# Kernel tuning notes

Measured on AMD Instinct MI355X. Metric: run time of the kernel, lower is better.

## Reference

```python
import jax, jax.numpy as jnp
import numpy as np

N = 50000      # nodes per type
E = 800000     # edges per relation
D = 128        # input feature dim
H = 128        # hidden_channels


def setup_inputs() -> dict:
    key = jax.random.key(0)
    ks = jax.random.split(key, 20)
    f = lambda k, shp: jax.random.normal(k, shp, dtype=jnp.float32) * 0.05
    inp = {
        "x_ligand": jax.random.normal(ks[0], (N, D), dtype=jnp.float32),
        "x_protein": jax.random.normal(ks[1], (N, D), dtype=jnp.float32),
        "ei_lp": jax.random.randint(ks[2], (2, E), 0, N, dtype=jnp.int64),
        "ei_pp": jax.random.randint(ks[3], (2, E), 0, N, dtype=jnp.int64),
        "ei_ll": jax.random.randint(ks[4], (2, E), 0, N, dtype=jnp.int64),
        "Wl_lp": f(ks[5], (D, H)), "bl_lp": f(ks[6], (H,)), "Wr_lp": f(ks[7], (D, H)),
        "Wl_pp": f(ks[8], (D, H)), "bl_pp": f(ks[9], (H,)), "Wr_pp": f(ks[10], (D, H)),
        "Wl_ll": f(ks[11], (D, H)), "bl_ll": f(ks[12], (H,)), "Wr_ll": f(ks[13], (D, H)),
        "W_out": f(ks[14], (H, 1)), "b_out": f(ks[15], (1,)),
    }
    return inp


def _sage(x_src, x_dst, edge_index, Wl, bl, Wr):
    # PyG SAGEConv: mean-aggregate neighbor (src) features onto dst, then
    # out = lin_l(agg) + lin_r(x_dst)  (lin_l has bias, lin_r does not)
    src, dst = edge_index[0], edge_index[1]
    n_dst = x_dst.shape[0]
    msgs = x_src[src]                                      # [E, D] gather
    s = jax.ops.segment_sum(msgs, dst, num_segments=n_dst) # [N_dst, D]
    cnt = jax.ops.segment_sum(jnp.ones((edge_index.shape[1],), x_src.dtype),
                              dst, num_segments=n_dst)     # [N_dst]
    agg = s / jnp.maximum(cnt, 1.0)[:, None]               # mean, 0 if isolated
    return agg @ Wl + bl + x_dst @ Wr


def reference(x_ligand, x_protein, ei_lp, ei_pp, ei_ll,
              Wl_lp, bl_lp, Wr_lp, Wl_pp, bl_pp, Wr_pp,
              Wl_ll, bl_ll, Wr_ll, W_out, b_out):
    # HeteroConv: sum contributions per destination node type
    protein_out = (_sage(x_ligand, x_protein, ei_lp, Wl_lp, bl_lp, Wr_lp)
                   + _sage(x_protein, x_protein, ei_pp, Wl_pp, bl_pp, Wr_pp))
    ligand_out = _sage(x_ligand, x_ligand, ei_ll, Wl_ll, bl_ll, Wr_ll)
    # relu per node type; only ligand is used downstream
    lig = jax.nn.relu(ligand_out).mean(axis=0)             # [H]
    _ = jax.nn.relu(protein_out)                           # computed in original
    return lig @ W_out + b_out                             # [1]
```

## Files before the change

### kernel.cpp

```cpp
#include <hip/hip_runtime.h>
#include <hip/hip_bf16.h>

#define DIM 128
#define EPB 4096
#define NRBIN 1024
#define RCAP 1280

typedef __attribute__((ext_vector_type(8))) short bf16x8;
typedef __attribute__((ext_vector_type(4))) float f32x4;
typedef __attribute__((ext_vector_type(4))) short short4v;
typedef __attribute__((ext_vector_type(4))) int int4v;

__device__ inline unsigned short f2bf(float f) {
  union { float f; unsigned u; } v; v.f = f;
  return (unsigned short)((v.u + 0x7FFFu + ((v.u >> 16) & 1u)) >> 16);
}
__device__ inline float lo_f(unsigned u) {
  union { unsigned u; float f; } v; v.u = u << 16; return v.f;
}
__device__ inline float hi_f(unsigned u) {
  union { unsigned u; float f; } v; v.u = u & 0xFFFF0000u; return v.f;
}

__global__ __launch_bounds__(256) void prep_part_kernel(
    const int* __restrict__ ei, unsigned* __restrict__ chunkbuf,
    int* __restrict__ startsT, int* __restrict__ countsT, int E, int nchunk,
    const float* __restrict__ x, short* __restrict__ A,
    const float* __restrict__ Wl, const float* __restrict__ Wr,
    short* __restrict__ Bpack, int nnodes, int mpad, int xb) {
  __shared__ unsigned uns[EPB];
  __shared__ unsigned srt[EPB];
  __shared__ int lhist[NRBIN];
  __shared__ int lstart[NRBIN];
  __shared__ int tsum[256];
  const int tid = threadIdx.x;
  const int bid = blockIdx.x;

  if (bid >= nchunk) {
    if (bid < nchunk + xb) {
      int t = (bid - nchunk) * 256 + tid;
      int node = t >> 5;
      if (node >= mpad) return;
      int c = (t & 31) * 4;
      short4v o = (short4v){0, 0, 0, 0};
      if (node < nnodes) {
        float4 v = *reinterpret_cast<const float4*>(x + (size_t)node * DIM + c);
        o.x = (short)f2bf(v.x); o.y = (short)f2bf(v.y);
        o.z = (short)f2bf(v.z); o.w = (short)f2bf(v.w);
      }
      *reinterpret_cast<short4v*>(A + (size_t)node * DIM + c) = o;
    } else {
      int t = (bid - nchunk - xb) * 256 + tid;
      if (t >= 4096) return;
      int lane = t & 63, nt = (t >> 6) & 7, ks = t >> 9;
      int c = nt * 16 + (lane & 15);
      int kb = ks * 32 + ((lane >> 4) << 3);
      bf16x8 o;
#pragma unroll
      for (int j = 0; j < 8; ++j) {
        int k = kb + j;
        float v = (k < DIM) ? Wl[k * DIM + c] : Wr[(k - DIM) * DIM + c];
        o[j] = (short)f2bf(v);
      }
      reinterpret_cast<bf16x8*>(Bpack)[(ks * 8 + nt) * 64 + lane] = o;
    }
    return;
  }

  const int chunk = bid;
  const int base = chunk * EPB;
  const int count = min(EPB, E - base);

#pragma unroll
  for (int r = 0; r < NRBIN / 256; ++r) lhist[tid + 256 * r] = 0;
  __syncthreads();

  for (int r = 0; r < EPB / 1024; ++r) {
    int i = r * 1024 + tid * 4;
    if (i + 3 < count) {
      int4 s4 = *reinterpret_cast<const int4*>(ei + base + i);
      int4 d4 = *reinterpret_cast<const int4*>(ei + E + base + i);
      int ss[4] = {s4.x, s4.y, s4.z, s4.w};
      int dd[4] = {d4.x, d4.y, d4.z, d4.w};
#pragma unroll
      for (int k = 0; k < 4; ++k) {
        unsigned reg = (unsigned)dd[k] >> 6;
        uns[i + k] = (reg << 22) | ((unsigned)(dd[k] & 63) << 16) | (unsigned)ss[k];
        atomicAdd(&lhist[reg], 1);
      }
    } else {
      for (int k = 0; k < 4; ++k) {
        if (i + k < count) {
          int s = ei[base + i + k], d = ei[E + base + i + k];
          unsigned reg = (unsigned)d >> 6;
          uns[i + k] = (reg << 22) | ((unsigned)(d & 63) << 16) | (unsigned)s;
          atomicAdd(&lhist[reg], 1);
        }
      }
    }
  }
  __syncthreads();

  int h0 = lhist[tid * 4], h1 = lhist[tid * 4 + 1];
  int h2 = lhist[tid * 4 + 2], h3 = lhist[tid * 4 + 3];
  int local = h0 + h1 + h2 + h3;
  tsum[tid] = local;
  __syncthreads();
  for (int o = 1; o < 256; o <<= 1) {
    int t = (tid >= o) ? tsum[tid - o] : 0;
    __syncthreads();
    tsum[tid] += t;
    __syncthreads();
  }
  int tb = tsum[tid] - local;
  lstart[tid * 4]     = tb;
  lstart[tid * 4 + 1] = tb + h0;
  lstart[tid * 4 + 2] = tb + h0 + h1;
  lstart[tid * 4 + 3] = tb + h0 + h1 + h2;
  lhist[tid * 4] = 0; lhist[tid * 4 + 1] = 0;
  lhist[tid * 4 + 2] = 0; lhist[tid * 4 + 3] = 0;
  __syncthreads();

  for (int i = tid; i < count; i += 256) {
    unsigned e = uns[i];
    unsigned reg = e >> 22;
    int pos = lstart[reg] + atomicAdd(&lhist[reg], 1);
    srt[pos] = e;
  }
  __syncthreads();

  for (int r = 0; r < EPB / 1024; ++r) {
    int i = r * 1024 + tid * 4;
    if (i + 3 < count) {
      int4v v = {(int)srt[i], (int)srt[i + 1], (int)srt[i + 2], (int)srt[i + 3]};
      *reinterpret_cast<int4v*>(chunkbuf + (size_t)chunk * EPB + i) = v;
    } else {
      for (int k = 0; k < 4; ++k)
        if (i + k < count) chunkbuf[(size_t)chunk * EPB + i + k] = srt[i + k];
    }
  }
  for (int r = tid; r < NRBIN; r += 256) {
    startsT[(size_t)chunk * NRBIN + r] = lstart[r];
    countsT[(size_t)chunk * NRBIN + r] = lhist[r];
  }
}

__global__ __launch_bounds__(256) void compact_kernel(
    const unsigned* __restrict__ chunkbuf, const int* __restrict__ startsT,
    const int* __restrict__ countsT, int nchunk, unsigned* __restrict__ csr,
    int* __restrict__ cnt, int* __restrict__ off) {
  __shared__ unsigned raw[RCAP];
  __shared__ unsigned srt[RCAP];
  __shared__ int h[64];
  __shared__ int start[64];
  __shared__ int tsum[256];
  const int region = blockIdx.x;
  const int tid = threadIdx.x;

  int cn = 0, st = 0;
  if (tid < nchunk) {
    cn = countsT[(size_t)tid * NRBIN + region];
    st = startsT[(size_t)tid * NRBIN + region];
  }
  tsum[tid] = cn;
  __syncthreads();
  for (int o = 1; o < 256; o <<= 1) {
    int t = (tid >= o) ? tsum[tid - o] : 0;
    __syncthreads();
    tsum[tid] += t;
    __syncthreads();
  }
  const int pfx = tsum[tid] - cn;
  int total = min(tsum[255], RCAP);

  const unsigned* src = chunkbuf + (size_t)tid * EPB + st;
  for (int j = 0; j < cn && pfx + j < RCAP; ++j) raw[pfx + j] = src[j];
  if (tid < 64) h[tid] = 0;
  __syncthreads();

  for (int i = tid; i < total; i += 256) atomicAdd(&h[(raw[i] >> 16) & 63], 1);
  __syncthreads();
  if (tid == 0) {
    int s = 0;
    for (int i = 0; i < 64; ++i) { start[i] = s; s += h[i]; }
  }
  __syncthreads();
  if (tid < 64) {
    int node = region * 64 + tid;
    cnt[node] = h[tid];
    off[node] = region * RCAP + start[tid];
    h[tid] = 0;
  }
  __syncthreads();
  for (int i = tid; i < total; i += 256) {
    unsigned e = raw[i];
    int d = (e >> 16) & 63;
    int pos = start[d] + atomicAdd(&h[d], 1);
    srt[pos] = e & 0xFFFFu;
  }
  __syncthreads();
  for (int i = tid; i < total; i += 256) csr[(size_t)region * RCAP + i] = srt[i];
}

__global__ __launch_bounds__(512) void aggmm_kernel(
    const int* __restrict__ cnt, const int* __restrict__ off,
    const unsigned* __restrict__ bucket, const short* __restrict__ A,
    const short* __restrict__ Bpack, const float* __restrict__ bl,
    float* __restrict__ partial, int nnodes) {
  __shared__ short a_lds[64 * 256];
  const int tid = threadIdx.x;
  const int wave = tid >> 6;
  const int lane = tid & 63;
  const int mt = blockIdx.x;
  const unsigned* xs = reinterpret_cast<const unsigned*>(A) + lane;

  for (int n = 0; n < 8; ++n) {
    const int row = wave * 8 + n;
    const int node = mt * 64 + row;
    float l0 = 0.f, h0 = 0.f, l1 = 0.f, h1 = 0.f;
    float r = 0.f;
    if (node < nnodes) {
      const int deg  = __builtin_amdgcn_readfirstlane(cnt[node]);
      const int base = __builtin_amdgcn_readfirstlane(off[node]);
      unsigned ent = (lane < deg) ? bucket[base + lane] : 0u;
      const int dcap = min(deg, 64);
      int j = 0;
      for (; j + 15 < dcap; j += 16) {
        unsigned u[16];
#pragma unroll
        for (int k = 0; k < 16; ++k) {
          int s = __builtin_amdgcn_readlane((int)ent, j + k);
          u[k] = xs[(size_t)s * 64];
        }
#pragma unroll
        for (int k = 0; k < 16; ++k) {
          if (k & 1) { l1 += lo_f(u[k]); h1 += hi_f(u[k]); }
          else       { l0 += lo_f(u[k]); h0 += hi_f(u[k]); }
        }
      }
      for (; j + 7 < dcap; j += 8) {
        unsigned u[8];
#pragma unroll
        for (int k = 0; k < 8; ++k) {
          int s = __builtin_amdgcn_readlane((int)ent, j + k);
          u[k] = xs[(size_t)s * 64];
        }
#pragma unroll
        for (int k = 0; k < 8; ++k) {
          if (k & 1) { l1 += lo_f(u[k]); h1 += hi_f(u[k]); }
          else       { l0 += lo_f(u[k]); h0 += hi_f(u[k]); }
        }
      }
      for (; j < dcap; ++j) {
        int s = __builtin_amdgcn_readlane((int)ent, j);
        unsigned u0 = xs[(size_t)s * 64];
        l0 += lo_f(u0); h0 += hi_f(u0);
      }
      for (; j < deg; ++j) {
        int s = __builtin_amdgcn_readfirstlane((int)bucket[base + j]);
        unsigned u0 = xs[(size_t)s * 64];
        l0 += lo_f(u0); h0 += hi_f(u0);
      }
      r = 1.0f / fmaxf((float)deg, 1.0f);
    }
    const unsigned o = (unsigned)f2bf((l0 + l1) * r) |
                       ((unsigned)f2bf((h0 + h1) * r) << 16);
    int byte = ((row * 512 + (lane >> 2) * 16) ^ ((row & 7) << 4)) + (lane & 3) * 4;
    *reinterpret_cast<unsigned*>(reinterpret_cast<char*>(a_lds) + byte) = o;
  }

#pragma unroll
  for (int rr = 0; rr < 2; ++rr) {
    int i = tid + 512 * rr;
    int row = i >> 4;
    int kc = 16 + (i & 15);
    bf16x8 v = *reinterpret_cast<const bf16x8*>(
        A + (size_t)(mt * 64 + row) * DIM + (kc - 16) * 8);
    int byte = (row * 512 + kc * 16) ^ ((row & 7) << 4);
    *reinterpret_cast<bf16x8*>(reinterpret_cast<char*>(a_lds) + byte) = v;
  }
  __syncthreads();

  f32x4 acc[4];
#pragma unroll
  for (int nt = 0; nt < 4; ++nt) acc[nt] = (f32x4){0.f, 0.f, 0.f, 0.f};

  const int stripe = wave >> 1;
  const int ntbase = (wave & 1) * 4;
  const int arow = stripe * 16 + (lane & 15);
  const int kgrp = lane >> 4;
  const bf16x8* Bp = reinterpret_cast<const bf16x8*>(Bpack);

#pragma unroll
  for (int ks = 0; ks < 8; ++ks) {
    int byte = (arow * 512 + (ks * 32 + kgrp * 8) * 2) ^ ((arow & 7) << 4);
    bf16x8 a = *reinterpret_cast<const bf16x8*>(reinterpret_cast<char*>(a_lds) + byte);
#pragma unroll
    for (int nt = 0; nt < 4; ++nt) {
      bf16x8 b = Bp[(ks * 8 + ntbase + nt) * 64 + lane];
      acc[nt] = __builtin_amdgcn_mfma_f32_16x16x32_bf16(a, b, acc[nt], 0, 0, 0);
    }
  }

  const int col16 = lane & 15;
  const int rowbase = mt * 64 + stripe * 16 + kgrp * 4;
#pragma unroll
  for (int nt = 0; nt < 4; ++nt) {
    const int c = (ntbase + nt) * 16 + col16;
    const float bb = bl[c];
    float s = 0.f;
#pragma unroll
    for (int rg = 0; rg < 4; ++rg) {
      float v = fmaxf(acc[nt][rg] + bb, 0.f);
      s += (rowbase + rg < nnodes) ? v : 0.f;
    }
    s += __shfl_xor(s, 16);
    s += __shfl_xor(s, 32);
    if (kgrp == 0) partial[((size_t)mt * 4 + stripe) * DIM + c] = s;
  }
}

__global__ __launch_bounds__(256) void red1_kernel(
    const float* __restrict__ partial, int nrows, float* __restrict__ red) {
  __shared__ float tmp[128];
  const int c = threadIdx.x & 127;
  const int half = threadIdx.x >> 7;
  const int chunk = (nrows + 127) / 128;
  const int r0 = blockIdx.x * chunk;
  const int r1 = min(r0 + chunk, nrows);
  float s = 0.f;
  for (int r = r0 + half; r < r1; r += 2) s += partial[(size_t)r * DIM + c];
  if (half) tmp[c] = s;
  __syncthreads();
  if (!half) red[(size_t)blockIdx.x * DIM + c] = s + tmp[c];
}

__global__ __launch_bounds__(256) void red2_kernel(
    const float* __restrict__ red, const float* __restrict__ Wout,
    const float* __restrict__ bout, float* __restrict__ out, int nnodes) {
  __shared__ float tmp[128];
  __shared__ float prod[128];
  const int c = threadIdx.x & 127;
  const int half = threadIdx.x >> 7;
  float s = 0.f;
  for (int r = half; r < 128; r += 2) s += red[(size_t)r * DIM + c];
  if (half) tmp[c] = s;
  __syncthreads();
  if (!half) prod[c] = (s + tmp[c]) * Wout[c];
  __syncthreads();
  if (threadIdx.x == 0) {
    float v = 0.f;
    for (int i = 0; i < 128; ++i) v += prod[i];
    out[0] = v / (float)nnodes + bout[0];
  }
}

extern "C" void kernel_launch(void* const* d_in, const int* in_sizes, int n_in,
                              void* d_out, int out_size, void* d_ws, size_t ws_size,
                              hipStream_t stream) {
  const float* x    = (const float*)d_in[0];
  const int*   ei   = (const int*)d_in[4];
  const float* Wl   = (const float*)d_in[11];
  const float* bl   = (const float*)d_in[12];
  const float* Wr   = (const float*)d_in[13];
  const float* Wout = (const float*)d_in[14];
  const float* bout = (const float*)d_in[15];

  const int nnodes = in_sizes[0] / DIM;
  const int E = in_sizes[4] / 2;
  const int mtiles = (nnodes + 63) / 64;
  const int mpad = mtiles * 64;
  const int nchunk = (E + EPB - 1) / EPB;

  unsigned* chunkbuf = (unsigned*)d_ws;
  int*      startsT  = (int*)(chunkbuf + (size_t)nchunk * EPB);
  int*      countsT  = startsT + (size_t)nchunk * NRBIN;
  unsigned* csr      = (unsigned*)(countsT + (size_t)nchunk * NRBIN);
  int*      cnt      = (int*)(csr + (size_t)mtiles * RCAP);
  int*      off      = cnt + mpad;
  short*    A        = (short*)(off + mpad);
  short*    Bpack    = A + (size_t)mpad * DIM;
  float*    red      = (float*)(Bpack + 32768);
  float*    partial  = (float*)chunkbuf;

  const int xb = mpad / 8;
  prep_part_kernel<<<nchunk + xb + 16, 256, 0, stream>>>(
      ei, chunkbuf, startsT, countsT, E, nchunk,
      x, A, Wl, Wr, Bpack, nnodes, mpad, xb);

  compact_kernel<<<mtiles, 256, 0, stream>>>(chunkbuf, startsT, countsT, nchunk,
                                             csr, cnt, off);

  aggmm_kernel<<<mtiles, 512, 0, stream>>>(cnt, off, csr, A, Bpack, bl,
                                           partial, nnodes);

  red1_kernel<<<128, 256, 0, stream>>>(partial, mtiles * 4, red);
  red2_kernel<<<1, 256, 0, stream>>>(red, Wout, bout, (float*)d_out, nnodes);
}
```

Before: 88.34 us.

## Use 1024-thread blocks in aggmm with 4 nodes per wave and batched metadata loads

Doubles the aggregation+matmul block to 16 waves so each wave gathers neighbor features for 4 destination nodes instead of 8. Each wave now loads all 4 nodes' degree/offset and CSR entries up front, so the latency of those dependent loads overlaps rather than being serialized per node. The MFMA stage is re-split so each wave computes 2 output column tiles instead of 4. The aim is more memory-level parallelism for the latency-bound gather. The cost is higher register pressure under the 1024-thread launch bound and possibly fewer resident blocks per CU.

```diff
diff --git a/kernel.cpp b/kernel.cpp
--- a/kernel.cpp
+++ b/kernel.cpp
@@ -202,7 +202,7 @@
   for (int i = tid; i < total; i += 256) csr[(size_t)region * RCAP + i] = srt[i];
 }
 
-__global__ __launch_bounds__(512) void aggmm_kernel(
+__global__ __launch_bounds__(1024) void aggmm_kernel(
     const int* __restrict__ cnt, const int* __restrict__ off,
     const unsigned* __restrict__ bucket, const short* __restrict__ A,
     const short* __restrict__ Bpack, const float* __restrict__ bl,
@@ -214,66 +214,76 @@
   const int mt = blockIdx.x;
   const unsigned* xs = reinterpret_cast<const unsigned*>(A) + lane;
 
-  for (int n = 0; n < 8; ++n) {
-    const int row = wave * 8 + n;
-    const int node = mt * 64 + row;
+  const int nb = mt * 64 + wave * 4;
+  int cv = 0, ov = 0;
+  if (lane < 4 && nb + lane < nnodes) {
+    cv = cnt[nb + lane];
+    ov = off[nb + lane];
+  }
+  int degs[4], bases[4];
+#pragma unroll
+  for (int n = 0; n < 4; ++n) {
+    degs[n]  = __builtin_amdgcn_readlane(cv, n);
+    bases[n] = __builtin_amdgcn_readlane(ov, n);
+  }
+  unsigned ents[4];
+#pragma unroll
+  for (int n = 0; n < 4; ++n)
+    ents[n] = (lane < degs[n]) ? bucket[bases[n] + lane] : 0u;
+
+#pragma unroll
+  for (int n = 0; n < 4; ++n) {
+    const int row = wave * 4 + n;
+    const int deg = degs[n];
+    const int dcap = min(deg, 64);
     float l0 = 0.f, h0 = 0.f, l1 = 0.f, h1 = 0.f;
-    float r = 0.f;
-    if (node < nnodes) {
-      const int deg  = __builtin_amdgcn_readfirstlane(cnt[node]);
-      const int base = __builtin_amdgcn_readfirstlane(off[node]);
-      unsigned ent = (lane < deg) ? bucket[base + lane] : 0u;
-      const int dcap = min(deg, 64);
-      int j = 0;
-      for (; j + 15 < dcap; j += 16) {
-        unsigned u[16];
-#pragma unroll
-        for (int k = 0; k < 16; ++k) {
-          int s = __builtin_amdgcn_readlane((int)ent, j + k);
-          u[k] = xs[(size_t)s * 64];
-        }
-#pragma unroll
-        for (int k = 0; k < 16; ++k) {
-          if (k & 1) { l1 += lo_f(u[k]); h1 += hi_f(u[k]); }
-          else       { l0 += lo_f(u[k]); h0 += hi_f(u[k]); }
-        }
-      }
-      for (; j + 7 < dcap; j += 8) {
-        unsigned u[8];
-#pragma unroll
-        for (int k = 0; k < 8; ++k) {
-          int s = __builtin_amdgcn_readlane((int)ent, j + k);
-          u[k] = xs[(size_t)s * 64];
-        }
-#pragma unroll
-        for (int k = 0; k < 8; ++k) {
-          if (k & 1) { l1 += lo_f(u[k]); h1 += hi_f(u[k]); }
-          else       { l0 += lo_f(u[k]); h0 += hi_f(u[k]); }
-        }
-      }
-      for (; j < dcap; ++j) {
-        int s = __builtin_amdgcn_readlane((int)ent, j);
-        unsigned u0 = xs[(size_t)s * 64];
-        l0 += lo_f(u0); h0 += hi_f(u0);
-      }
-      for (; j < deg; ++j) {
-        int s = __builtin_amdgcn_readfirstlane((int)bucket[base + j]);
-        unsigned u0 = xs[(size_t)s * 64];
-        l0 += lo_f(u0); h0 += hi_f(u0);
-      }
-      r = 1.0f / fmaxf((float)deg, 1.0f);
-    }
+    int j = 0;
+    for (; j + 15 < dcap; j += 16) {
+      unsigned u[16];
+#pragma unroll
+      for (int k = 0; k < 16; ++k) {
+        int s = __builtin_amdgcn_readlane((int)ents[n], j + k);
+        u[k] = xs[(size_t)s * 64];
+      }
+#pragma unroll
+      for (int k = 0; k < 16; ++k) {
+        if (k & 1) { l1 += lo_f(u[k]); h1 += hi_f(u[k]); }
+        else       { l0 += lo_f(u[k]); h0 += hi_f(u[k]); }
+      }
+    }
+    for (; j + 7 < dcap; j += 8) {
+      unsigned u[8];
+#pragma unroll
+      for (int k = 0; k < 8; ++k) {
+        int s = __builtin_amdgcn_readlane((int)ents[n], j + k);
+        u[k] = xs[(size_t)s * 64];
+      }
+#pragma unroll
+      for (int k = 0; k < 8; ++k) {
+        if (k & 1) { l1 += lo_f(u[k]); h1 += hi_f(u[k]); }
+        else       { l0 += lo_f(u[k]); h0 += hi_f(u[k]); }
+      }
+    }
+    for (; j < dcap; ++j) {
+      int s = __builtin_amdgcn_readlane((int)ents[n], j);
+      unsigned u0 = xs[(size_t)s * 64];
+      l0 += lo_f(u0); h0 += hi_f(u0);
+    }
+    for (; j < deg; ++j) {
+      int s = __builtin_amdgcn_readfirstlane((int)bucket[bases[n] + j]);
+      unsigned u0 = xs[(size_t)s * 64];
+      l0 += lo_f(u0); h0 += hi_f(u0);
+    }
+    const float r = (nb + n < nnodes) ? 1.0f / fmaxf((float)deg, 1.0f) : 0.f;
     const unsigned o = (unsigned)f2bf((l0 + l1) * r) |
                        ((unsigned)f2bf((h0 + h1) * r) << 16);
     int byte = ((row * 512 + (lane >> 2) * 16) ^ ((row & 7) << 4)) + (lane & 3) * 4;
     *reinterpret_cast<unsigned*>(reinterpret_cast<char*>(a_lds) + byte) = o;
   }
 
-#pragma unroll
-  for (int rr = 0; rr < 2; ++rr) {
-    int i = tid + 512 * rr;
-    int row = i >> 4;
-    int kc = 16 + (i & 15);
+  {
+    int row = tid >> 4;
+    int kc = 16 + (tid & 15);
     bf16x8 v = *reinterpret_cast<const bf16x8*>(
         A + (size_t)(mt * 64 + row) * DIM + (kc - 16) * 8);
     int byte = (row * 512 + kc * 16) ^ ((row & 7) << 4);
@@ -281,12 +291,12 @@
   }
   __syncthreads();
 
-  f32x4 acc[4];
-#pragma unroll
-  for (int nt = 0; nt < 4; ++nt) acc[nt] = (f32x4){0.f, 0.f, 0.f, 0.f};
-
-  const int stripe = wave >> 1;
-  const int ntbase = (wave & 1) * 4;
+  f32x4 acc[2];
+#pragma unroll
+  for (int nt = 0; nt < 2; ++nt) acc[nt] = (f32x4){0.f, 0.f, 0.f, 0.f};
+
+  const int stripe = wave >> 2;
+  const int ntbase = (wave & 3) * 2;
   const int arow = stripe * 16 + (lane & 15);
   const int kgrp = lane >> 4;
   const bf16x8* Bp = reinterpret_cast<const bf16x8*>(Bpack);
@@ -296,7 +306,7 @@
     int byte = (arow * 512 + (ks * 32 + kgrp * 8) * 2) ^ ((arow & 7) << 4);
     bf16x8 a = *reinterpret_cast<const bf16x8*>(reinterpret_cast<char*>(a_lds) + byte);
 #pragma unroll
-    for (int nt = 0; nt < 4; ++nt) {
+    for (int nt = 0; nt < 2; ++nt) {
       bf16x8 b = Bp[(ks * 8 + ntbase + nt) * 64 + lane];
       acc[nt] = __builtin_amdgcn_mfma_f32_16x16x32_bf16(a, b, acc[nt], 0, 0, 0);
     }
@@ -305,7 +315,7 @@
   const int col16 = lane & 15;
   const int rowbase = mt * 64 + stripe * 16 + kgrp * 4;
 #pragma unroll
-  for (int nt = 0; nt < 4; ++nt) {
+  for (int nt = 0; nt < 2; ++nt) {
     const int c = (ntbase + nt) * 16 + col16;
     const float bb = bl[c];
     float s = 0.f;
@@ -391,8 +401,8 @@
   compact_kernel<<<mtiles, 256, 0, stream>>>(chunkbuf, startsT, countsT, nchunk,
                                              csr, cnt, off);
 
-  aggmm_kernel<<<mtiles, 512, 0, stream>>>(cnt, off, csr, A, Bpack, bl,
-                                           partial, nnodes);
+  aggmm_kernel<<<mtiles, 1024, 0, stream>>>(cnt, off, csr, A, Bpack, bl,
+                                            partial, nnodes);
 
   red1_kernel<<<128, 256, 0, stream>>>(partial, mtiles * 4, red);
   red2_kernel<<<1, 256, 0, stream>>>(red, Wout, bout, (float*)d_out, nnodes);
```

After: 88.23 us. No clear change (-0.1%).
